# Performance work log

Measured on AMD Instinct MI355X. Metric: run time of the kernel, lower is better.

## Reference

```python
import jax, jax.numpy as jnp
import numpy as np

N, Fdim, Aout = 8192, 32, 8
AVG_DEG = 32.0  # target average degree for the random graph


def setup_inputs() -> dict:
    key = jax.random.key(0)
    ks = jax.random.split(key, 12)
    x = jax.random.normal(ks[0], (N, Fdim), dtype=jnp.float32)
    # binary adjacency, zero diagonal (GCNConv adds self-loops itself)
    u = jax.random.uniform(ks[1], (N, N), dtype=jnp.float32)
    adj = (u < (AVG_DEG / N)).astype(jnp.float32)
    adj = adj * (1.0 - jnp.eye(N, dtype=jnp.float32))
    mask = (jax.random.uniform(ks[2], (N,), dtype=jnp.float32) < 0.5).astype(jnp.float32)

    def lin(k, fout, fin):
        s = 1.0 / np.sqrt(fin)
        return jax.random.uniform(k, (fout, fin), jnp.float32, -s, s)

    return {
        "x": x, "adj": adj, "mask": mask,
        "w1": lin(ks[3], 64, Fdim), "b1": jnp.zeros((64,), jnp.float32),
        "w2": lin(ks[4], 128, 64), "b2": jnp.zeros((128,), jnp.float32),
        "wg": lin(ks[5], 128, 128), "bg": jnp.zeros((128,), jnp.float32),
        "wd": lin(ks[6], 128, 128), "bd": jnp.zeros((128,), jnp.float32),
        "wp1": lin(ks[7], 128, 256), "bp1": jnp.zeros((128,), jnp.float32),
        "wp2": lin(ks[8], 64, 128), "bp2": jnp.zeros((64,), jnp.float32),
        "wo": lin(ks[9], Aout, 64), "bo": jnp.zeros((Aout,), jnp.float32),
    }


def reference(x, adj, mask, w1, b1, w2, b2, wg, bg, wd, bd, wp1, bp1, wp2, bp2, wo, bo):
    # encoder MLP
    h = jax.nn.relu(x @ w1.T + b1)           # [N,64]
    h = jax.nn.relu(h @ w2.T + b2)           # [N,128]
    # GCNConv with default self-loops and symmetric normalization:
    # out = D^{-1/2} (A + I) D^{-1/2} (h W^T) + b
    a_hat = adj + jnp.eye(adj.shape[0], dtype=adj.dtype)
    deg = jnp.sum(a_hat, axis=1)             # >= 1 thanks to self-loops
    dinv = jax.lax.rsqrt(deg)
    msg = h @ wg.T                            # [N,128]
    agg = dinv[:, None] * (a_hat @ (dinv[:, None] * msg))  # normalized aggregation
    g = jax.nn.relu(agg + bg)
    g = jax.nn.relu(g @ wd.T + bd)
    f = jnp.concatenate([g, h], axis=1)       # [N,256]
    p = jax.nn.relu(f @ wp1.T + bp1)
    p = jax.nn.relu(p @ wp2.T + bp2)
    out = (p @ wo.T + bo) * mask[:, None]     # [N,Aout]
    return out
```

## Files before the change

### kernel.cpp

```cpp
#include <hip/hip_runtime.h>

#define N_NODES 8192
#define CAP 128
#define ETILE 16
#define DTILE 8
constexpr int AST = 132;
constexpr int WST = 129;

typedef unsigned u32x4 __attribute__((ext_vector_type(4)));

__global__ __launch_bounds__(256, 4) void scan_kernel(
    const float* __restrict__ adj, int* __restrict__ cnt,
    int* __restrict__ nbr) {
  const int t = threadIdx.x;
  const int lane = t & 63;
  const int row = blockIdx.x * 4 + (t >> 6);
  const u32x4* rowp = (const u32x4*)(adj + (size_t)row * N_NODES);
  u32x4 v[8], vn[8];
#pragma unroll
  for (int i = 0; i < 8; ++i) v[i] = __builtin_nontemporal_load(&rowp[i * 64 + lane]);
  int running = 0;
  int* nbr_row = nbr + (size_t)row * CAP;
  for (int ch = 0; ch < 4; ++ch) {
    if (ch < 3) {
      const u32x4* cp = rowp + (ch + 1) * 512;
#pragma unroll
      for (int i = 0; i < 8; ++i) vn[i] = __builtin_nontemporal_load(&cp[i * 64 + lane]);
    }
    int c = 0;
#pragma unroll
    for (int i = 0; i < 8; ++i)
      c += (v[i].x != 0u) + (v[i].y != 0u) + (v[i].z != 0u) + (v[i].w != 0u);
    int incl = c;
#pragma unroll
    for (int s = 1; s < 64; s <<= 1) {
      int n = __shfl_up(incl, s);
      if (lane >= s) incl += n;
    }
    int off = running + incl - c;
    running += __shfl(incl, 63);
    const int colbase = ch * 2048;
#pragma unroll
    for (int i = 0; i < 8; ++i) {
      if (v[i].x | v[i].y | v[i].z | v[i].w) {
        const int col = colbase + (i * 64 + lane) * 4;
        if (v[i].x) { if (off < CAP) nbr_row[off] = col + 0; ++off; }
        if (v[i].y) { if (off < CAP) nbr_row[off] = col + 1; ++off; }
        if (v[i].z) { if (off < CAP) nbr_row[off] = col + 2; ++off; }
        if (v[i].w) { if (off < CAP) nbr_row[off] = col + 3; ++off; }
      }
    }
#pragma unroll
    for (int i = 0; i < 8; ++i) v[i] = vn[i];
  }
  if (lane == 0) cnt[row] = running;
}

template <int TILE, int K, int KSPLIT, int F, bool RELU, bool BIAS, int SCALEMODE>
__device__ __forceinline__ void layer_op(
    const float (*__restrict__ A0)[AST], const float (*__restrict__ A1)[AST],
    float (*__restrict__ Aout)[AST], float (*__restrict__ Wb)[WST],
    const float* __restrict__ W, const float* __restrict__ bias,
    float* __restrict__ gout, const float* __restrict__ rowscale,
    const int* __restrict__ degcnt, int n0, int t) {
  constexpr int KC = 32;
  constexpr int NCH = K / KC;
  constexpr int ACT = (F * TILE < 256) ? F * TILE : 256;
  constexpr int RS = ACT / F;
  constexpr int RPT = TILE / RS;
  const int c = t % F;
  const int rb = t / F;
  float acc[RPT];
#pragma unroll
  for (int i = 0; i < RPT; ++i) acc[i] = 0.f;

  for (int ch = 0; ch < NCH; ++ch) {
#pragma unroll
    for (int i = 0; i < (F * KC + 255) / 256; ++i) {
      int lin = t + i * 256;
      if ((F * KC) % 256 == 0 || lin < F * KC) {
        int k = lin % KC, f = lin / KC;
        Wb[k][f] = W[(size_t)f * K + ch * KC + k];
      }
    }
    __syncthreads();
    if (t < ACT) {
      const float (*__restrict__ As)[AST] = (ch * KC < KSPLIT) ? A0 : A1;
      const int kb = (ch * KC < KSPLIT) ? ch * KC : ch * KC - KSPLIT;
#pragma unroll
      for (int kg = 0; kg < KC / 4; ++kg) {
        float w0 = Wb[kg * 4 + 0][c];
        float w1v = Wb[kg * 4 + 1][c];
        float w2v = Wb[kg * 4 + 2][c];
        float w3v = Wb[kg * 4 + 3][c];
#pragma unroll
        for (int i = 0; i < RPT; ++i) {
          const float4 a = *(const float4*)&As[rb + i * RS][kb + kg * 4];
          acc[i] = fmaf(a.x, w0, acc[i]);
          acc[i] = fmaf(a.y, w1v, acc[i]);
          acc[i] = fmaf(a.z, w2v, acc[i]);
          acc[i] = fmaf(a.w, w3v, acc[i]);
        }
      }
    }
    __syncthreads();
  }
  if (t < ACT) {
#pragma unroll
    for (int i = 0; i < RPT; ++i) {
      float v = acc[i];
      if (BIAS) v += bias[c];
      if (RELU) v = fmaxf(v, 0.f);
      int node = n0 + rb + i * RS;
      if (SCALEMODE == 1) v *= rowscale[node];
      if (SCALEMODE == 2) v *= rsqrtf((float)degcnt[node] + 1.0f);
      if (Aout) Aout[rb + i * RS][c] = v;
      if (gout) gout[(size_t)node * F + c] = v;
    }
  }
}

__global__ __launch_bounds__(256) void encode_kernel(
    const float* __restrict__ x,
    const float* __restrict__ w1, const float* __restrict__ b1,
    const float* __restrict__ w2, const float* __restrict__ b2,
    const float* __restrict__ wg, const int* __restrict__ cnt,
    float* __restrict__ h_out, float* __restrict__ msg_out) {
  __shared__ float bufA[ETILE][AST];
  __shared__ float bufB[ETILE][AST];
  __shared__ float Wb[32][WST];
  const int t = threadIdx.x;
  const int n0 = blockIdx.x * ETILE;
  if (t < 128) {
    int row = t >> 3, k4 = (t & 7) * 4;
    *(float4*)&bufA[row][k4] = *(const float4*)&x[(size_t)(n0 + row) * 32 + k4];
  }
  layer_op<ETILE, 32, 32, 64, true, true, 0>(bufA, nullptr, bufB, Wb, w1, b1, nullptr, nullptr, nullptr, n0, t);
  layer_op<ETILE, 64, 64, 128, true, true, 0>(bufB, nullptr, bufA, Wb, w2, b2, h_out, nullptr, nullptr, n0, t);
  layer_op<ETILE, 128, 128, 128, false, false, 2>(bufA, nullptr, nullptr, Wb, wg, nullptr, msg_out, nullptr, cnt, n0, t);
}

__global__ __launch_bounds__(256) void agg_kernel(
    const int* __restrict__ cnt, const int* __restrict__ nbr,
    const float* __restrict__ msg, const float* __restrict__ bg,
    const float* __restrict__ adj, float* __restrict__ g1) {
  const int t = threadIdx.x;
  const int f = t & 127;
  const int rA = blockIdx.x * 4 + (t >> 7) * 2;
  const int rB = rA + 1;
  const int cA = cnt[rA], cB = cnt[rB];
  float a0 = msg[(size_t)rA * 128 + f];
  float a1 = msg[(size_t)rB * 128 + f];
  if (cA <= CAP && cB <= CAP) {
    const int* nA = nbr + (size_t)rA * CAP;
    const int* nB = nbr + (size_t)rB * CAP;
    const int cm = max(cA, cB);
    for (int i = 0; i < cm; i += 4) {
#pragma unroll
      for (int k = 0; k < 4; ++k) {
        const int ii = i + k;
        int jA = nA[ii < cA ? ii : 0] & (N_NODES - 1);
        int jB = nB[ii < cB ? ii : 0] & (N_NODES - 1);
        float vA = msg[(size_t)jA * 128 + f];
        float vB = msg[(size_t)jB * 128 + f];
        a0 += (ii < cA) ? vA : 0.f;
        a1 += (ii < cB) ? vB : 0.f;
      }
    }
  } else {
    a0 = msg[(size_t)rA * 128 + f];
    a1 = msg[(size_t)rB * 128 + f];
    for (int col = 0; col < N_NODES; ++col) {
      if (adj[(size_t)rA * N_NODES + col] != 0.f) a0 += msg[(size_t)col * 128 + f];
      if (adj[(size_t)rB * N_NODES + col] != 0.f) a1 += msg[(size_t)col * 128 + f];
    }
  }
  float o0 = fmaf(rsqrtf((float)cA + 1.0f), a0, bg[f]);
  float o1 = fmaf(rsqrtf((float)cB + 1.0f), a1, bg[f]);
  g1[(size_t)rA * 128 + f] = fmaxf(o0, 0.f);
  g1[(size_t)rB * 128 + f] = fmaxf(o1, 0.f);
}

__global__ __launch_bounds__(256) void decode_kernel(
    const float* __restrict__ g1, const float* __restrict__ h,
    const float* __restrict__ wd, const float* __restrict__ bd,
    const float* __restrict__ wp1, const float* __restrict__ bp1,
    const float* __restrict__ wp2, const float* __restrict__ bp2,
    const float* __restrict__ wo, const float* __restrict__ bo,
    const float* __restrict__ mask, float* __restrict__ out) {
  __shared__ float bufA[DTILE][AST];
  __shared__ float bufB[DTILE][AST];
  __shared__ float bufH[DTILE][AST];
  __shared__ float Wb[32][WST];
  const int t = threadIdx.x;
  const int n0 = blockIdx.x * DTILE;
  {
    int row = t >> 5, k4 = (t & 31) * 4;
    *(float4*)&bufA[row][k4] = *(const float4*)&g1[(size_t)(n0 + row) * 128 + k4];
    *(float4*)&bufH[row][k4] = *(const float4*)&h[(size_t)(n0 + row) * 128 + k4];
  }
  layer_op<DTILE, 128, 128, 128, true, true, 0>(bufA, nullptr, bufB, Wb, wd, bd, nullptr, nullptr, nullptr, n0, t);
  layer_op<DTILE, 256, 128, 128, true, true, 0>(bufB, bufH, bufA, Wb, wp1, bp1, nullptr, nullptr, nullptr, n0, t);
  layer_op<DTILE, 128, 128, 64, true, true, 0>(bufA, nullptr, bufB, Wb, wp2, bp2, nullptr, nullptr, nullptr, n0, t);
  layer_op<DTILE, 64, 64, 8, false, true, 1>(bufB, nullptr, nullptr, Wb, wo, bo, out, mask, nullptr, n0, t);
}

extern "C" void kernel_launch(void* const* d_in, const int* in_sizes, int n_in,
                              void* d_out, int out_size, void* d_ws, size_t ws_size,
                              hipStream_t stream) {
  const float* x    = (const float*)d_in[0];
  const float* adj  = (const float*)d_in[1];
  const float* mask = (const float*)d_in[2];
  const float* w1   = (const float*)d_in[3];
  const float* b1   = (const float*)d_in[4];
  const float* w2   = (const float*)d_in[5];
  const float* b2   = (const float*)d_in[6];
  const float* wg   = (const float*)d_in[7];
  const float* bg   = (const float*)d_in[8];
  const float* wd   = (const float*)d_in[9];
  const float* bd   = (const float*)d_in[10];
  const float* wp1  = (const float*)d_in[11];
  const float* bp1  = (const float*)d_in[12];
  const float* wp2  = (const float*)d_in[13];
  const float* bp2  = (const float*)d_in[14];
  const float* wo   = (const float*)d_in[15];
  const float* bo   = (const float*)d_in[16];
  float* out = (float*)d_out;

  float* ws = (float*)d_ws;
  float* h    = ws; ws += (size_t)N_NODES * 128;
  float* msg  = ws; ws += (size_t)N_NODES * 128;
  float* g1   = ws; ws += (size_t)N_NODES * 128;
  int* cnt = (int*)ws; ws += N_NODES;
  int* nbr = (int*)ws;

  scan_kernel<<<N_NODES / 4, 256, 0, stream>>>(adj, cnt, nbr);
  encode_kernel<<<N_NODES / ETILE, 256, 0, stream>>>(x, w1, b1, w2, b2, wg, cnt, h, msg);
  agg_kernel<<<N_NODES / 4, 256, 0, stream>>>(cnt, nbr, msg, bg, adj, g1);
  decode_kernel<<<N_NODES / DTILE, 256, 0, stream>>>(
      g1, h, wd, bd, wp1, bp1, wp2, bp2, wo, bo, mask, out);
}
```

Before: 454.8 us.

## Fuse scan with encoder and aggregation with decoder into two kernels

Result: slower. 505.6 us (+11.2%).

```diff
diff --git a/kernel.cpp b/kernel.cpp
--- a/kernel.cpp
+++ b/kernel.cpp
@@ -9,60 +9,13 @@
 
 typedef unsigned u32x4 __attribute__((ext_vector_type(4)));
 
-__global__ __launch_bounds__(256, 4) void scan_kernel(
-    const float* __restrict__ adj, int* __restrict__ cnt,
-    int* __restrict__ nbr) {
-  const int t = threadIdx.x;
-  const int lane = t & 63;
-  const int row = blockIdx.x * 4 + (t >> 6);
-  const u32x4* rowp = (const u32x4*)(adj + (size_t)row * N_NODES);
-  u32x4 v[8], vn[8];
-#pragma unroll
-  for (int i = 0; i < 8; ++i) v[i] = __builtin_nontemporal_load(&rowp[i * 64 + lane]);
-  int running = 0;
-  int* nbr_row = nbr + (size_t)row * CAP;
-  for (int ch = 0; ch < 4; ++ch) {
-    if (ch < 3) {
-      const u32x4* cp = rowp + (ch + 1) * 512;
-#pragma unroll
-      for (int i = 0; i < 8; ++i) vn[i] = __builtin_nontemporal_load(&cp[i * 64 + lane]);
-    }
-    int c = 0;
-#pragma unroll
-    for (int i = 0; i < 8; ++i)
-      c += (v[i].x != 0u) + (v[i].y != 0u) + (v[i].z != 0u) + (v[i].w != 0u);
-    int incl = c;
-#pragma unroll
-    for (int s = 1; s < 64; s <<= 1) {
-      int n = __shfl_up(incl, s);
-      if (lane >= s) incl += n;
-    }
-    int off = running + incl - c;
-    running += __shfl(incl, 63);
-    const int colbase = ch * 2048;
-#pragma unroll
-    for (int i = 0; i < 8; ++i) {
-      if (v[i].x | v[i].y | v[i].z | v[i].w) {
-        const int col = colbase + (i * 64 + lane) * 4;
-        if (v[i].x) { if (off < CAP) nbr_row[off] = col + 0; ++off; }
-        if (v[i].y) { if (off < CAP) nbr_row[off] = col + 1; ++off; }
-        if (v[i].z) { if (off < CAP) nbr_row[off] = col + 2; ++off; }
-        if (v[i].w) { if (off < CAP) nbr_row[off] = col + 3; ++off; }
-      }
-    }
-#pragma unroll
-    for (int i = 0; i < 8; ++i) v[i] = vn[i];
-  }
-  if (lane == 0) cnt[row] = running;
-}
-
 template <int TILE, int K, int KSPLIT, int F, bool RELU, bool BIAS, int SCALEMODE>
 __device__ __forceinline__ void layer_op(
     const float (*__restrict__ A0)[AST], const float (*__restrict__ A1)[AST],
     float (*__restrict__ Aout)[AST], float (*__restrict__ Wb)[WST],
     const float* __restrict__ W, const float* __restrict__ bias,
     float* __restrict__ gout, const float* __restrict__ rowscale,
-    const int* __restrict__ degcnt, int n0, int t) {
+    int n0, int t) {
   constexpr int KC = 32;
   constexpr int NCH = K / KC;
   constexpr int ACT = (F * TILE < 256) ? F * TILE : 256;
@@ -113,76 +66,94 @@
       if (RELU) v = fmaxf(v, 0.f);
       int node = n0 + rb + i * RS;
       if (SCALEMODE == 1) v *= rowscale[node];
-      if (SCALEMODE == 2) v *= rsqrtf((float)degcnt[node] + 1.0f);
       if (Aout) Aout[rb + i * RS][c] = v;
       if (gout) gout[(size_t)node * F + c] = v;
     }
   }
 }
 
-__global__ __launch_bounds__(256) void encode_kernel(
+__global__ __launch_bounds__(256) void fused_scan_encode_kernel(
+    const float* __restrict__ adj, int* __restrict__ cnt,
+    float* __restrict__ dinv, int* __restrict__ nbr,
     const float* __restrict__ x,
     const float* __restrict__ w1, const float* __restrict__ b1,
     const float* __restrict__ w2, const float* __restrict__ b2,
-    const float* __restrict__ wg, const int* __restrict__ cnt,
+    const float* __restrict__ wg,
     float* __restrict__ h_out, float* __restrict__ msg_out) {
   __shared__ float bufA[ETILE][AST];
   __shared__ float bufB[ETILE][AST];
   __shared__ float Wb[32][WST];
   const int t = threadIdx.x;
-  const int n0 = blockIdx.x * ETILE;
-  if (t < 128) {
-    int row = t >> 3, k4 = (t & 7) * 4;
-    *(float4*)&bufA[row][k4] = *(const float4*)&x[(size_t)(n0 + row) * 32 + k4];
-  }
-  layer_op<ETILE, 32, 32, 64, true, true, 0>(bufA, nullptr, bufB, Wb, w1, b1, nullptr, nullptr, nullptr, n0, t);
-  layer_op<ETILE, 64, 64, 128, true, true, 0>(bufB, nullptr, bufA, Wb, w2, b2, h_out, nullptr, nullptr, n0, t);
-  layer_op<ETILE, 128, 128, 128, false, false, 2>(bufA, nullptr, nullptr, Wb, wg, nullptr, msg_out, nullptr, cnt, n0, t);
-}
-
-__global__ __launch_bounds__(256) void agg_kernel(
-    const int* __restrict__ cnt, const int* __restrict__ nbr,
-    const float* __restrict__ msg, const float* __restrict__ bg,
-    const float* __restrict__ adj, float* __restrict__ g1) {
-  const int t = threadIdx.x;
-  const int f = t & 127;
-  const int rA = blockIdx.x * 4 + (t >> 7) * 2;
-  const int rB = rA + 1;
-  const int cA = cnt[rA], cB = cnt[rB];
-  float a0 = msg[(size_t)rA * 128 + f];
-  float a1 = msg[(size_t)rB * 128 + f];
-  if (cA <= CAP && cB <= CAP) {
-    const int* nA = nbr + (size_t)rA * CAP;
-    const int* nB = nbr + (size_t)rB * CAP;
-    const int cm = max(cA, cB);
-    for (int i = 0; i < cm; i += 4) {
-#pragma unroll
-      for (int k = 0; k < 4; ++k) {
-        const int ii = i + k;
-        int jA = nA[ii < cA ? ii : 0] & (N_NODES - 1);
-        int jB = nB[ii < cB ? ii : 0] & (N_NODES - 1);
-        float vA = msg[(size_t)jA * 128 + f];
-        float vB = msg[(size_t)jB * 128 + f];
-        a0 += (ii < cA) ? vA : 0.f;
-        a1 += (ii < cB) ? vB : 0.f;
-      }
+  const int q = blockIdx.x / 5;
+  const int r5 = blockIdx.x % 5;
+
+  if (r5 < 4) {
+    const int lane = t & 63;
+    const int row = (q * 4 + r5) * 4 + (t >> 6);
+    const u32x4* rowp = (const u32x4*)(adj + (size_t)row * N_NODES);
+    const int p0 = row & 3;
+    u32x4 v[8], vn[8];
+    {
+      const u32x4* cp = rowp + p0 * 512;
+#pragma unroll
+      for (int i = 0; i < 8; ++i) v[i] = __builtin_nontemporal_load(&cp[i * 64 + lane]);
+    }
+    int running = 0;
+    int* nbr_row = nbr + (size_t)row * CAP;
+    for (int ci = 0; ci < 4; ++ci) {
+      const int cur = (p0 + ci) & 3;
+      if (ci < 3) {
+        const u32x4* cp = rowp + (((p0 + ci + 1) & 3) * 512);
+#pragma unroll
+        for (int i = 0; i < 8; ++i) vn[i] = __builtin_nontemporal_load(&cp[i * 64 + lane]);
+      }
+      int c = 0;
+#pragma unroll
+      for (int i = 0; i < 8; ++i)
+        c += (v[i].x != 0u) + (v[i].y != 0u) + (v[i].z != 0u) + (v[i].w != 0u);
+      int incl = c;
+#pragma unroll
+      for (int s = 1; s < 64; s <<= 1) {
+        int n = __shfl_up(incl, s);
+        if (lane >= s) incl += n;
+      }
+      int off = running + incl - c;
+      running += __shfl(incl, 63);
+      const int colbase = cur * 2048;
+#pragma unroll
+      for (int i = 0; i < 8; ++i) {
+        if (v[i].x | v[i].y | v[i].z | v[i].w) {
+          const int col = colbase + (i * 64 + lane) * 4;
+          if (v[i].x) { if (off < CAP) nbr_row[off] = col + 0; ++off; }
+          if (v[i].y) { if (off < CAP) nbr_row[off] = col + 1; ++off; }
+          if (v[i].z) { if (off < CAP) nbr_row[off] = col + 2; ++off; }
+          if (v[i].w) { if (off < CAP) nbr_row[off] = col + 3; ++off; }
+        }
+      }
+#pragma unroll
+      for (int i = 0; i < 8; ++i) v[i] = vn[i];
+    }
+    if (lane == 0) {
+      cnt[row] = running;
+      dinv[row] = rsqrtf((float)running + 1.0f);
     }
   } else {
-    a0 = msg[(size_t)rA * 128 + f];
-    a1 = msg[(size_t)rB * 128 + f];
-    for (int col = 0; col < N_NODES; ++col) {
-      if (adj[(size_t)rA * N_NODES + col] != 0.f) a0 += msg[(size_t)col * 128 + f];
-      if (adj[(size_t)rB * N_NODES + col] != 0.f) a1 += msg[(size_t)col * 128 + f];
-    }
-  }
-  float o0 = fmaf(rsqrtf((float)cA + 1.0f), a0, bg[f]);
-  float o1 = fmaf(rsqrtf((float)cB + 1.0f), a1, bg[f]);
-  g1[(size_t)rA * 128 + f] = fmaxf(o0, 0.f);
-  g1[(size_t)rB * 128 + f] = fmaxf(o1, 0.f);
-}
-
-__global__ __launch_bounds__(256) void decode_kernel(
-    const float* __restrict__ g1, const float* __restrict__ h,
+    const int n0 = q * ETILE;
+    if (t < 128) {
+      int row = t >> 3, k4 = (t & 7) * 4;
+      *(float4*)&bufA[row][k4] = *(const float4*)&x[(size_t)(n0 + row) * 32 + k4];
+    }
+    layer_op<ETILE, 32, 32, 64, true, true, 0>(bufA, nullptr, bufB, Wb, w1, b1, nullptr, nullptr, n0, t);
+    layer_op<ETILE, 64, 64, 128, true, true, 0>(bufB, nullptr, bufA, Wb, w2, b2, h_out, nullptr, n0, t);
+    layer_op<ETILE, 128, 128, 128, false, false, 0>(bufA, nullptr, nullptr, Wb, wg, nullptr, msg_out, nullptr, n0, t);
+  }
+}
+
+__global__ __launch_bounds__(256) void agg_decode_kernel(
+    const int* __restrict__ cnt, const float* __restrict__ dinv,
+    const int* __restrict__ nbr, const float* __restrict__ msg,
+    const float* __restrict__ adj, const float* __restrict__ h,
+    const float* __restrict__ bg,
     const float* __restrict__ wd, const float* __restrict__ bd,
     const float* __restrict__ wp1, const float* __restrict__ bp1,
     const float* __restrict__ wp2, const float* __restrict__ bp2,
@@ -196,13 +167,54 @@
   const int n0 = blockIdx.x * DTILE;
   {
     int row = t >> 5, k4 = (t & 31) * 4;
-    *(float4*)&bufA[row][k4] = *(const float4*)&g1[(size_t)(n0 + row) * 128 + k4];
     *(float4*)&bufH[row][k4] = *(const float4*)&h[(size_t)(n0 + row) * 128 + k4];
   }
-  layer_op<DTILE, 128, 128, 128, true, true, 0>(bufA, nullptr, bufB, Wb, wd, bd, nullptr, nullptr, nullptr, n0, t);
-  layer_op<DTILE, 256, 128, 128, true, true, 0>(bufB, bufH, bufA, Wb, wp1, bp1, nullptr, nullptr, nullptr, n0, t);
-  layer_op<DTILE, 128, 128, 64, true, true, 0>(bufA, nullptr, bufB, Wb, wp2, bp2, nullptr, nullptr, nullptr, n0, t);
-  layer_op<DTILE, 64, 64, 8, false, true, 1>(bufB, nullptr, nullptr, Wb, wo, bo, out, mask, nullptr, n0, t);
+  const int f = t & 127;
+  const int g = t >> 7;
+  const int rbase = n0 + g * 4;
+  int c[4];
+  float dv[4], acc[4];
+  const int* np[4];
+  bool ok = true;
+#pragma unroll
+  for (int k = 0; k < 4; ++k) {
+    const int r = rbase + k;
+    c[k] = cnt[r];
+    dv[k] = dinv[r];
+    np[k] = nbr + (size_t)r * CAP;
+    acc[k] = dv[k] * msg[(size_t)r * 128 + f];
+    ok = ok && (c[k] <= CAP);
+  }
+  if (ok) {
+    const int cm = max(max(c[0], c[1]), max(c[2], c[3]));
+    for (int i = 0; i < cm; i += 2) {
+#pragma unroll
+      for (int m = 0; m < 2; ++m) {
+#pragma unroll
+        for (int k = 0; k < 4; ++k) {
+          const int ii = i + m;
+          const int j = np[k][ii < c[k] ? ii : 0] & (N_NODES - 1);
+          const float w = (ii < c[k]) ? dinv[j] : 0.f;
+          acc[k] = fmaf(w, msg[(size_t)j * 128 + f], acc[k]);
+        }
+      }
+    }
+  } else {
+#pragma unroll
+    for (int k = 0; k < 4; ++k) {
+      const int r = rbase + k;
+      for (int col = 0; col < N_NODES; ++col)
+        if (adj[(size_t)r * N_NODES + col] != 0.f)
+          acc[k] += dinv[col] * msg[(size_t)col * 128 + f];
+    }
+  }
+#pragma unroll
+  for (int k = 0; k < 4; ++k)
+    bufA[g * 4 + k][f] = fmaxf(fmaf(dv[k], acc[k], bg[f]), 0.f);
+  layer_op<DTILE, 128, 128, 128, true, true, 0>(bufA, nullptr, bufB, Wb, wd, bd, nullptr, nullptr, n0, t);
+  layer_op<DTILE, 256, 128, 128, true, true, 0>(bufB, bufH, bufA, Wb, wp1, bp1, nullptr, nullptr, n0, t);
+  layer_op<DTILE, 128, 128, 64, true, true, 0>(bufA, nullptr, bufB, Wb, wp2, bp2, nullptr, nullptr, n0, t);
+  layer_op<DTILE, 64, 64, 8, false, true, 1>(bufB, nullptr, nullptr, Wb, wo, bo, out, mask, n0, t);
 }
 
 extern "C" void kernel_launch(void* const* d_in, const int* in_sizes, int n_in,
@@ -230,13 +242,12 @@
   float* ws = (float*)d_ws;
   float* h    = ws; ws += (size_t)N_NODES * 128;
   float* msg  = ws; ws += (size_t)N_NODES * 128;
-  float* g1   = ws; ws += (size_t)N_NODES * 128;
+  float* dinv = ws; ws += N_NODES;
   int* cnt = (int*)ws; ws += N_NODES;
   int* nbr = (int*)ws;
 
-  scan_kernel<<<N_NODES / 4, 256, 0, stream>>>(adj, cnt, nbr);
-  encode_kernel<<<N_NODES / ETILE, 256, 0, stream>>>(x, w1, b1, w2, b2, wg, cnt, h, msg);
-  agg_kernel<<<N_NODES / 4, 256, 0, stream>>>(cnt, nbr, msg, bg, adj, g1);
-  decode_kernel<<<N_NODES / DTILE, 256, 0, stream>>>(
-      g1, h, wd, bd, wp1, bp1, wp2, bp2, wo, bo, mask, out);
-}
+  fused_scan_encode_kernel<<<2560, 256, 0, stream>>>(
+      adj, cnt, dinv, nbr, x, w1, b1, w2, b2, wg, h, msg);
+  agg_decode_kernel<<<N_NODES / DTILE, 256, 0, stream>>>(
+      cnt, dinv, nbr, msg, adj, h, bg, wd, bd, wp1, bp1, wp2, bp2, wo, bo, mask, out);
+}
```

## Run decoder MLP on MFMA with split-bf16 weights pre-packed in fragment layout

Applied to the files above, without the earlier changes.

Result: faster. 430.6 us (-5.3%).

```diff
diff --git a/kernel.cpp b/kernel.cpp
--- a/kernel.cpp
+++ b/kernel.cpp
@@ -3,11 +3,19 @@
 #define N_NODES 8192
 #define CAP 128
 #define ETILE 16
-#define DTILE 8
 constexpr int AST = 132;
 constexpr int WST = 129;
 
 typedef unsigned u32x4 __attribute__((ext_vector_type(4)));
+typedef unsigned short u16;
+typedef __attribute__((ext_vector_type(8))) short bf16x8;
+typedef __attribute__((ext_vector_type(4))) float f32x4;
+
+constexpr size_t OFF_WD = 0;
+constexpr size_t OFF_WP1 = 16384;
+constexpr size_t OFF_WP2 = 49152;
+constexpr size_t OFF_WO = 57344;
+constexpr size_t WTOT = 58368;
 
 __global__ __launch_bounds__(256, 4) void scan_kernel(
     const float* __restrict__ adj, int* __restrict__ cnt,
@@ -181,28 +189,117 @@
   g1[(size_t)rB * 128 + f] = fmaxf(o1, 0.f);
 }
 
-__global__ __launch_bounds__(256) void decode_kernel(
+__global__ __launch_bounds__(256) void prep_weights(
+    const float* __restrict__ wd, const float* __restrict__ wp1,
+    const float* __restrict__ wp2, const float* __restrict__ wo,
+    u16* __restrict__ bh, u16* __restrict__ bl) {
+  const int gid = blockIdx.x * 256 + threadIdx.x;
+  if (gid >= (int)WTOT) return;
+  const float* W; int K, F; size_t off; int rel; bool pad = false;
+  if (gid < 16384)      { W = wd;  K = 128; F = 128; off = OFF_WD;  rel = gid; }
+  else if (gid < 49152) { W = wp1; K = 256; F = 128; off = OFF_WP1; rel = gid - 16384; }
+  else if (gid < 57344) { W = wp2; K = 128; F = 64;  off = OFF_WP2; rel = gid - 49152; }
+  else                  { W = wo;  K = 64;  F = 16;  off = OFF_WO;  rel = gid - 57344; pad = true; }
+  const int j = rel & 7, lane = (rel >> 3) & 63, t2 = rel >> 9;
+  const int nf = F >> 4;
+  const int ftile = t2 % nf, kstep = t2 / nf;
+  const int k = kstep * 32 + ((lane >> 4) << 3) + j;
+  const int f = ftile * 16 + (lane & 15);
+  const float v = (pad && f >= 8) ? 0.f : W[(size_t)f * K + k];
+  const unsigned u = __float_as_uint(v);
+  const unsigned uh = u & 0xffff0000u;
+  const float r = v - __uint_as_float(uh);
+  bh[off + rel] = (u16)(uh >> 16);
+  bl[off + rel] = (u16)(__float_as_uint(r) >> 16);
+}
+
+template <int K, int F, int KSPLIT, bool RELU, bool FINAL>
+__device__ __forceinline__ void mfma_layer(
+    const float (*__restrict__ A0)[AST], const float (*__restrict__ A1)[AST],
+    const u16* __restrict__ Bh, const u16* __restrict__ Bl,
+    const float* __restrict__ bias, float (*__restrict__ O)[AST],
+    float* __restrict__ gout, const float* __restrict__ mask,
+    int nbase, int lane) {
+  constexpr int NK = K / 32, NF = F / 16;
+  f32x4 acc[NF];
+  const f32x4 zz = {0.f, 0.f, 0.f, 0.f};
+#pragma unroll
+  for (int i = 0; i < NF; ++i) acc[i] = zz;
+  const int arow = lane & 15;
+  const int kgrp = (lane >> 4) << 3;
+#pragma unroll
+  for (int ks = 0; ks < NK; ++ks) {
+    const float* ap = (ks * 32 < KSPLIT) ? &A0[arow][ks * 32 + kgrp]
+                                         : &A1[arow][ks * 32 - KSPLIT + kgrp];
+    const float4 p0 = *(const float4*)ap;
+    const float4 p1 = *(const float4*)(ap + 4);
+    const float av[8] = {p0.x, p0.y, p0.z, p0.w, p1.x, p1.y, p1.z, p1.w};
+    bf16x8 ahi, alo;
+#pragma unroll
+    for (int j = 0; j < 8; ++j) {
+      const unsigned u = __float_as_uint(av[j]);
+      const unsigned uh = u & 0xffff0000u;
+      const float r = av[j] - __uint_as_float(uh);
+      ahi[j] = (short)(uh >> 16);
+      alo[j] = (short)(__float_as_uint(r) >> 16);
+    }
+#pragma unroll
+    for (int ft = 0; ft < NF; ++ft) {
+      const size_t idx = ((size_t)(ks * NF + ft) * 64 + lane) * 8;
+      const bf16x8 wh = *(const bf16x8*)(Bh + idx);
+      const bf16x8 wl = *(const bf16x8*)(Bl + idx);
+      acc[ft] = __builtin_amdgcn_mfma_f32_16x16x32_bf16(ahi, wh, acc[ft], 0, 0, 0);
+      acc[ft] = __builtin_amdgcn_mfma_f32_16x16x32_bf16(ahi, wl, acc[ft], 0, 0, 0);
+      acc[ft] = __builtin_amdgcn_mfma_f32_16x16x32_bf16(alo, wh, acc[ft], 0, 0, 0);
+    }
+  }
+#pragma unroll
+  for (int ft = 0; ft < NF; ++ft) {
+    const int f = ft * 16 + (lane & 15);
+    if (FINAL && f >= 8) continue;
+    const float bv = bias[f];
+#pragma unroll
+    for (int r = 0; r < 4; ++r) {
+      const int row = ((lane >> 4) << 2) + r;
+      float v = acc[ft][r] + bv;
+      if (RELU) v = fmaxf(v, 0.f);
+      if (!FINAL) O[row][f] = v;
+      else gout[(size_t)(nbase + row) * 8 + f] = v * mask[nbase + row];
+    }
+  }
+}
+
+__global__ __launch_bounds__(128) void mfma_decode(
     const float* __restrict__ g1, const float* __restrict__ h,
-    const float* __restrict__ wd, const float* __restrict__ bd,
-    const float* __restrict__ wp1, const float* __restrict__ bp1,
-    const float* __restrict__ wp2, const float* __restrict__ bp2,
-    const float* __restrict__ wo, const float* __restrict__ bo,
+    const u16* __restrict__ bh, const u16* __restrict__ bl,
+    const float* __restrict__ bd, const float* __restrict__ bp1,
+    const float* __restrict__ bp2, const float* __restrict__ bo,
     const float* __restrict__ mask, float* __restrict__ out) {
-  __shared__ float bufA[DTILE][AST];
-  __shared__ float bufB[DTILE][AST];
-  __shared__ float bufH[DTILE][AST];
-  __shared__ float Wb[32][WST];
+  __shared__ float actA[2][16][AST];
+  __shared__ float actB[2][16][AST];
+  __shared__ float actH[2][16][AST];
   const int t = threadIdx.x;
-  const int n0 = blockIdx.x * DTILE;
-  {
-    int row = t >> 5, k4 = (t & 31) * 4;
-    *(float4*)&bufA[row][k4] = *(const float4*)&g1[(size_t)(n0 + row) * 128 + k4];
-    *(float4*)&bufH[row][k4] = *(const float4*)&h[(size_t)(n0 + row) * 128 + k4];
-  }
-  layer_op<DTILE, 128, 128, 128, true, true, 0>(bufA, nullptr, bufB, Wb, wd, bd, nullptr, nullptr, nullptr, n0, t);
-  layer_op<DTILE, 256, 128, 128, true, true, 0>(bufB, bufH, bufA, Wb, wp1, bp1, nullptr, nullptr, nullptr, n0, t);
-  layer_op<DTILE, 128, 128, 64, true, true, 0>(bufA, nullptr, bufB, Wb, wp2, bp2, nullptr, nullptr, nullptr, n0, t);
-  layer_op<DTILE, 64, 64, 8, false, true, 1>(bufB, nullptr, nullptr, Wb, wo, bo, out, mask, nullptr, n0, t);
+  const int w = t >> 6, lane = t & 63;
+  const int n0 = blockIdx.x * 32 + w * 16;
+#pragma unroll
+  for (int i = 0; i < 8; ++i) {
+    const int fi = i * 64 + lane;
+    const int row = fi >> 5, c4 = (fi & 31) * 4;
+    *(float4*)&actA[w][row][c4] = *(const float4*)&g1[(size_t)(n0 + row) * 128 + c4];
+    *(float4*)&actH[w][row][c4] = *(const float4*)&h[(size_t)(n0 + row) * 128 + c4];
+  }
+  __syncthreads();
+  mfma_layer<128, 128, 128, true, false>(actA[w], actA[w], bh + OFF_WD, bl + OFF_WD,
+                                         bd, actB[w], nullptr, nullptr, n0, lane);
+  __syncthreads();
+  mfma_layer<256, 128, 128, true, false>(actB[w], actH[w], bh + OFF_WP1, bl + OFF_WP1,
+                                         bp1, actA[w], nullptr, nullptr, n0, lane);
+  __syncthreads();
+  mfma_layer<128, 64, 128, true, false>(actA[w], actA[w], bh + OFF_WP2, bl + OFF_WP2,
+                                        bp2, actB[w], nullptr, nullptr, n0, lane);
+  __syncthreads();
+  mfma_layer<64, 16, 128, false, true>(actB[w], actB[w], bh + OFF_WO, bl + OFF_WO,
+                                       bo, nullptr, out, mask, n0, lane);
 }
 
 extern "C" void kernel_launch(void* const* d_in, const int* in_sizes, int n_in,
@@ -232,11 +329,13 @@
   float* msg  = ws; ws += (size_t)N_NODES * 128;
   float* g1   = ws; ws += (size_t)N_NODES * 128;
   int* cnt = (int*)ws; ws += N_NODES;
-  int* nbr = (int*)ws;
-
+  int* nbr = (int*)ws; ws += (size_t)N_NODES * CAP;
+  u16* bh = (u16*)ws;
+  u16* bl = bh + WTOT;
+
+  prep_weights<<<(int)((WTOT + 255) / 256), 256, 0, stream>>>(wd, wp1, wp2, wo, bh, bl);
   scan_kernel<<<N_NODES / 4, 256, 0, stream>>>(adj, cnt, nbr);
   encode_kernel<<<N_NODES / ETILE, 256, 0, stream>>>(x, w1, b1, w2, b2, wg, cnt, h, msg);
   agg_kernel<<<N_NODES / 4, 256, 0, stream>>>(cnt, nbr, msg, bg, adj, g1);
-  decode_kernel<<<N_NODES / DTILE, 256, 0, stream>>>(
-      g1, h, wd, bd, wp1, bp1, wp2, bp2, wo, bo, mask, out);
-}
+  mfma_decode<<<N_NODES / 32, 128, 0, stream>>>(g1, h, bh, bl, bd, bp1, bp2, bo, mask, out);
+}
```
